# Optimization experiments

Hardware: AMD Instinct MI355X
Metric: run time of the kernel (lower is better)

The kernel has to match this reference:

```python
import jax, jax.numpy as jnp
import numpy as np

POOL = 7  # pool_size


def setup_inputs() -> dict:
    key = jax.random.key(0)
    k1, k2, k3, k4, k5 = jax.random.split(key, 5)
    H = W = 64
    C = 1024
    R = 1024  # num_rois
    img = jax.random.normal(k1, (1, H, W, C), dtype=jnp.float32)
    x = jax.random.randint(k2, (1, R), 0, W - 16)
    y = jax.random.randint(k3, (1, R), 0, H - 16)
    w = jax.random.randint(k4, (1, R), 1, 17)
    h = jax.random.randint(k5, (1, R), 1, 17)
    rois = jnp.stack([x, y, w, h], axis=-1).astype(jnp.int32)  # (1, R, 4)
    return {"img": img, "rois": rois}


def _axis_coords(start, size, pool):
    """Per-ROI bilinear source coords for tf.image.resize (half-pixel centers).
    start,size: (R,) int32. Returns absolute low/high indices (R,pool) int32
    and interpolation weight (R,pool) float32."""
    scale = size.astype(jnp.float32) / pool
    src = (jnp.arange(pool, dtype=jnp.float32) + 0.5)[None, :] * scale[:, None] - 0.5
    f = jnp.floor(src)
    lerp = src - f
    lo = jnp.clip(f.astype(jnp.int32), 0, size[:, None] - 1)
    hi = jnp.clip(f.astype(jnp.int32) + 1, 0, size[:, None] - 1)
    return start[:, None] + lo, start[:, None] + hi, lerp


def reference(img, rois):
    # img: (1, H, W, C); rois: (1, R, 4) int32 with (x, y, w, h)
    r = rois[0]
    x, y, w, h = r[:, 0], r[:, 1], r[:, 2], r[:, 3]
    y0, y1, ty = _axis_coords(y, h, POOL)  # (R, P)
    x0, x1, tx = _axis_coords(x, w, POOL)  # (R, P)
    im = img[0]  # (H, W, C)

    def gather(yy, xx):
        # (R, P, P, C) corner gather, vectorized over all ROIs
        return im[yy[:, :, None], xx[:, None, :], :]

    tx_ = tx[:, None, :, None]
    ty_ = ty[:, :, None, None]
    top = gather(y0, x0) * (1.0 - tx_) + gather(y0, x1) * tx_
    bot = gather(y1, x0) * (1.0 - tx_) + gather(y1, x1) * tx_
    out = top * (1.0 - ty_) + bot * ty_  # (R, P, P, C)
    return out[None]  # (1, R, P, P, C)
```

## Files before the change

kernel.cpp:

```cpp
#include <hip/hip_runtime.h>


#define POOLSZ 7
#define IMG_H 64
#define IMG_W 64
#define IMG_C 1024

__global__ __launch_bounds__(256) void roi_pool_kernel(
    const float* __restrict__ img,
    const int* __restrict__ rois,
    float* __restrict__ out) {
    const int cell = blockIdx.x;
    const int px = cell % POOLSZ;
    const int py = (cell / POOLSZ) % POOLSZ;
    const int r  = cell / (POOLSZ * POOLSZ);

    const int4 roi = ((const int4*)rois)[r];
    const int rx = roi.x, ry = roi.y, rw = roi.z, rh = roi.w;

    const float scy  = (float)rh * (1.0f / (float)POOLSZ);
    const float srcy = ((float)py + 0.5f) * scy - 0.5f;
    const float fy   = floorf(srcy);
    const float ty   = srcy - fy;
    const int   iy   = (int)fy;
    const int   y0   = ry + min(max(iy,     0), rh - 1);
    const int   y1   = ry + min(max(iy + 1, 0), rh - 1);

    const float scx  = (float)rw * (1.0f / (float)POOLSZ);
    const float srcx = ((float)px + 0.5f) * scx - 0.5f;
    const float fx   = floorf(srcx);
    const float tx   = srcx - fx;
    const int   ix   = (int)fx;
    const int   x0   = rx + min(max(ix,     0), rw - 1);
    const int   x1   = rx + min(max(ix + 1, 0), rw - 1);

    const int c4 = threadIdx.x;

    const float4* p00 = (const float4*)(img + ((size_t)y0 * IMG_W + x0) * IMG_C) + c4;
    const float4* p01 = (const float4*)(img + ((size_t)y0 * IMG_W + x1) * IMG_C) + c4;
    const float4* p10 = (const float4*)(img + ((size_t)y1 * IMG_W + x0) * IMG_C) + c4;
    const float4* p11 = (const float4*)(img + ((size_t)y1 * IMG_W + x1) * IMG_C) + c4;

    const float4 a = *p00;
    const float4 b = *p01;
    const float4 c = *p10;
    const float4 d = *p11;

    float4 top, bot, o;
    top.x = a.x + (b.x - a.x) * tx;
    top.y = a.y + (b.y - a.y) * tx;
    top.z = a.z + (b.z - a.z) * tx;
    top.w = a.w + (b.w - a.w) * tx;
    bot.x = c.x + (d.x - c.x) * tx;
    bot.y = c.y + (d.y - c.y) * tx;
    bot.z = c.z + (d.z - c.z) * tx;
    bot.w = c.w + (d.w - c.w) * tx;
    o.x = top.x + (bot.x - top.x) * ty;
    o.y = top.y + (bot.y - top.y) * ty;
    o.z = top.z + (bot.z - top.z) * ty;
    o.w = top.w + (bot.w - top.w) * ty;

    ((float4*)out)[(size_t)cell * (IMG_C / 4) + c4] = o;
}

extern "C" void kernel_launch(void* const* d_in, const int* in_sizes, int n_in,
                              void* d_out, int out_size, void* d_ws, size_t ws_size,
                              hipStream_t stream) {
    const float* img  = (const float*)d_in[0];
    const int*   rois = (const int*)d_in[1];
    float*       out  = (float*)d_out;
    const int R = in_sizes[1] / 4;
    const int n_cells = R * POOLSZ * POOLSZ;
    roi_pool_kernel<<<n_cells, 256, 0, stream>>>(img, rois, out);
}
```

Baseline: 254.8 us.

## Remap blocks so each XCD handles contiguous ROIs and use nontemporal stores

Blocks are remapped so that round-robin XCD dispatch places a contiguous chunk of ROIs on each XCD. Neighbouring cells of one ROI then share that XCD's L2 for the overlapping corner pixels. Output writes become nontemporal stores so the large write stream does less to evict the reused image data. The remap relies on an assumed XCD dispatch order and falls back to linear indexing when R is not a multiple of 8.

```diff
diff --git a/kernel.cpp b/kernel.cpp
--- a/kernel.cpp
+++ b/kernel.cpp
@@ -5,15 +5,27 @@
 #define IMG_H 64
 #define IMG_W 64
 #define IMG_C 1024
+#define NUM_XCD 8
+
+typedef float v4f __attribute__((ext_vector_type(4)));
 
 __global__ __launch_bounds__(256) void roi_pool_kernel(
     const float* __restrict__ img,
     const int* __restrict__ rois,
-    float* __restrict__ out) {
-    const int cell = blockIdx.x;
+    float* __restrict__ out,
+    int roisPerXcd) {
+    int r, cell;
+    if (roisPerXcd > 0) {
+        const int xcd   = blockIdx.x & (NUM_XCD - 1);
+        const int local = blockIdx.x >> 3;
+        r    = xcd * roisPerXcd + local / (POOLSZ * POOLSZ);
+        cell = local % (POOLSZ * POOLSZ);
+    } else {
+        r    = blockIdx.x / (POOLSZ * POOLSZ);
+        cell = blockIdx.x % (POOLSZ * POOLSZ);
+    }
     const int px = cell % POOLSZ;
-    const int py = (cell / POOLSZ) % POOLSZ;
-    const int r  = cell / (POOLSZ * POOLSZ);
+    const int py = cell / POOLSZ;
 
     const int4 roi = ((const int4*)rois)[r];
     const int rx = roi.x, ry = roi.y, rw = roi.z, rh = roi.w;
@@ -36,31 +48,22 @@
 
     const int c4 = threadIdx.x;
 
-    const float4* p00 = (const float4*)(img + ((size_t)y0 * IMG_W + x0) * IMG_C) + c4;
-    const float4* p01 = (const float4*)(img + ((size_t)y0 * IMG_W + x1) * IMG_C) + c4;
-    const float4* p10 = (const float4*)(img + ((size_t)y1 * IMG_W + x0) * IMG_C) + c4;
-    const float4* p11 = (const float4*)(img + ((size_t)y1 * IMG_W + x1) * IMG_C) + c4;
+    const v4f* p00 = (const v4f*)(img + ((size_t)y0 * IMG_W + x0) * IMG_C) + c4;
+    const v4f* p01 = (const v4f*)(img + ((size_t)y0 * IMG_W + x1) * IMG_C) + c4;
+    const v4f* p10 = (const v4f*)(img + ((size_t)y1 * IMG_W + x0) * IMG_C) + c4;
+    const v4f* p11 = (const v4f*)(img + ((size_t)y1 * IMG_W + x1) * IMG_C) + c4;
 
-    const float4 a = *p00;
-    const float4 b = *p01;
-    const float4 c = *p10;
-    const float4 d = *p11;
+    const v4f a = *p00;
+    const v4f b = *p01;
+    const v4f c = *p10;
+    const v4f d = *p11;
 
-    float4 top, bot, o;
-    top.x = a.x + (b.x - a.x) * tx;
-    top.y = a.y + (b.y - a.y) * tx;
-    top.z = a.z + (b.z - a.z) * tx;
-    top.w = a.w + (b.w - a.w) * tx;
-    bot.x = c.x + (d.x - c.x) * tx;
-    bot.y = c.y + (d.y - c.y) * tx;
-    bot.z = c.z + (d.z - c.z) * tx;
-    bot.w = c.w + (d.w - c.w) * tx;
-    o.x = top.x + (bot.x - top.x) * ty;
-    o.y = top.y + (bot.y - top.y) * ty;
-    o.z = top.z + (bot.z - top.z) * ty;
-    o.w = top.w + (bot.w - top.w) * ty;
+    const v4f top = a + (b - a) * tx;
+    const v4f bot = c + (d - c) * tx;
+    const v4f o   = top + (bot - top) * ty;
 
-    ((float4*)out)[(size_t)cell * (IMG_C / 4) + c4] = o;
+    v4f* dst = (v4f*)out + ((size_t)r * (POOLSZ * POOLSZ) + cell) * (IMG_C / 4) + c4;
+    __builtin_nontemporal_store(o, dst);
 }
 
 extern "C" void kernel_launch(void* const* d_in, const int* in_sizes, int n_in,
@@ -71,5 +74,6 @@
     float*       out  = (float*)d_out;
     const int R = in_sizes[1] / 4;
     const int n_cells = R * POOLSZ * POOLSZ;
-    roi_pool_kernel<<<n_cells, 256, 0, stream>>>(img, rois, out);
+    const int roisPerXcd = (R % NUM_XCD == 0) ? (R / NUM_XCD) : 0;
+    roi_pool_kernel<<<n_cells, 256, 0, stream>>>(img, rois, out, roisPerXcd);
 }
```

After: 241.2 us. 1.06x faster.
